# Optimization experiments

Hardware: AMD Instinct MI355X
Metric: run time of the kernel (lower is better)

## Reference

```python
import jax, jax.numpy as jnp
import numpy as np

ALPHA, BETA = 0.5, 0.25
DELTA_AGG, DELTA_DIS = 0.5, 3.0
OHEM_RATIO = 3
MAX_INST = 8  # instance ids in [0, MAX_INST); 0 = background
NEG_INF = -1e10


def _safe_norm(sq):
    # sqrt with zero-safe gradient; returns 0 where sq == 0
    return jnp.sqrt(jnp.where(sq > 0, sq, 1.0)) * (sq > 0)


def _agg_dis_single(sim, gt_text, gt_kernel):
    # sim: [4, N] float, gt_text/gt_kernel: [N] int32 instance ids
    lab = jnp.arange(1, MAX_INST)                                  # [K]
    kmask = (gt_kernel[None, :] == lab[:, None]).astype(sim.dtype)  # [K, N]
    tmask = gt_text[None, :] == lab[:, None]                        # [K, N] bool
    kcount = kmask.sum(1)
    tcount = tmask.sum(1).astype(sim.dtype)
    valid = (kcount > 0) & (tcount > 0)                             # [K]
    # per-instance kernel centroid G_kernel: masked segment mean of sim vectors
    G = (kmask @ sim.T) / jnp.maximum(kcount, 1.0)[:, None]         # [K, 4]
    # loss_agg: distance of each text pixel's sim vector to its kernel centroid
    diff = sim.T[None, :, :] - G[:, None, :]                        # [K, N, 4]
    d = _safe_norm(jnp.sum(diff * diff, -1))                        # [K, N]
    D = jnp.square(jnp.maximum(d - DELTA_AGG, 0.0))
    per_inst = jnp.sum(jnp.log1p(D) * tmask, 1) / jnp.maximum(tcount, 1.0)
    n_valid = jnp.sum(valid)
    loss_agg = jnp.sum(jnp.where(valid, per_inst, 0.0)) / jnp.maximum(n_valid, 1).astype(sim.dtype)
    # loss_dis: pairwise discrimination between valid kernel centroids
    gd = G[:, None, :] - G[None, :, :]                              # [K, K, 4]
    gnorm = _safe_norm(jnp.sum(gd * gd, -1))
    Dij = jnp.square(jnp.maximum(DELTA_DIS - gnorm, 0.0))
    K = MAX_INST - 1
    idx = jnp.arange(K)
    pair = valid[:, None] & valid[None, :] & (idx[:, None] < idx[None, :])
    s = jnp.sum(jnp.where(pair, jnp.log1p(Dij), 0.0))
    denom = (n_valid * (n_valid - 1)).astype(sim.dtype)  # matches torch: n*(n-1), not #pairs
    loss_dis = jnp.where(n_valid > 1, s / jnp.maximum(denom, 1.0), 0.0)
    return loss_agg, loss_dis


def _ohem_single(score, gt, tm):
    # score/tm: [N] float, gt: [N] int — all flattened
    pos = gt > 0.5
    pos_num = jnp.sum(pos) - jnp.sum(pos & (tm <= 0.5))
    neg = ~pos
    neg_total = jnp.sum(neg)
    neg_num = jnp.minimum(pos_num * OHEM_RATIO, neg_total)
    neg_scores = jnp.where(neg, score, NEG_INF)
    sorted_desc = -jnp.sort(-neg_scores)
    threshold = sorted_desc[jnp.maximum(neg_num - 1, 0)]
    sel = (((score >= threshold) | pos) & (tm > 0.5)).astype(tm.dtype)
    fallback = (pos_num == 0) | (neg_num == 0)
    return jnp.where(fallback, tm, sel)


def _dice(inp, tgt, mask):
    # inp: [B, N] logits, tgt: [B, N] (binarized at 0.5), mask: [B, N]
    p = jax.nn.sigmoid(inp) * mask
    t = (tgt > 0.5).astype(p.dtype) * mask
    a = jnp.sum(p * t, 1)
    b = jnp.sum(p * p, 1) + 1e-3
    c = jnp.sum(t * t, 1) + 1e-3
    return 1.0 - 2.0 * a / (b + c)


def _pan_loss(outputs, labels, training_masks):
    B = outputs.shape[0]
    texts = outputs[:, 0].reshape(B, -1)
    kernels = outputs[:, 1].reshape(B, -1)
    sim = outputs[:, 2:].reshape(B, 4, -1)
    gt_texts = labels[:, 0].reshape(B, -1)
    gt_kernels = labels[:, 1].reshape(B, -1)
    tm = training_masks.reshape(B, -1)

    loss_aggs, loss_diss = jax.vmap(_agg_dis_single)(sim, gt_texts, gt_kernels)

    # OHEM mask is computed on detached scores in the original (numpy round-trip)
    sel_text = jax.vmap(_ohem_single)(jax.lax.stop_gradient(texts), gt_texts, tm)
    loss_texts = _dice(texts, gt_texts, sel_text)

    sel_kernel = jax.lax.stop_gradient(
        ((jax.nn.sigmoid(texts) > 0.5) & (tm > 0.5)).astype(texts.dtype))
    loss_kernels = _dice(kernels, gt_kernels, sel_kernel)

    loss_text = loss_texts.mean()
    loss_kernel = loss_kernels.mean()
    loss_agg = loss_aggs.mean()
    loss_dis = loss_diss.mean()
    loss_all = loss_text + ALPHA * loss_kernel + BETA * (loss_agg + loss_dis)
    return loss_all, loss_text, loss_kernel, loss_agg, loss_dis


def setup_inputs() -> dict:
    key = jax.random.key(0)
    k1, k2, k3 = jax.random.split(key, 3)
    B, H, W = 8, 640, 640
    outputs = jax.random.normal(k1, (B, 6, H, W), dtype=jnp.float32)
    labels = jax.random.randint(k2, (B, 2, H, W), 0, MAX_INST).astype(jnp.int32)
    training_masks = jax.random.uniform(k3, (B, H, W), dtype=jnp.float32)
    return {"outputs": outputs, "labels": labels, "training_masks": training_masks}


def reference(outputs, labels, training_masks):
    return _pan_loss(outputs, labels, training_masks)
```

## Files before the change

kernel.cpp:

```cpp
#include <hip/hip_runtime.h>

#define NPIX 409600
#define NB 8

constexpr int OFF_H0   = 0;
constexpr int OFF_H1   = 2048;
constexpr int OFF_H2   = 4096;
constexpr int OFF_KC   = 5120;
constexpr int OFF_TC   = 5128;
constexpr int OFF_KS   = 5136;
constexpr int OFF_AGG  = 5168;
constexpr int OFF_CPOS = 5176;
constexpr int OFF_CPOSM= 5177;
constexpr int OFF_KN   = 5178;
constexpr int OFF_KNF  = 5179;
constexpr int OFF_FALL = 5180;
constexpr int OFF_NV   = 5181;
constexpr int OFF_VM   = 5182;
constexpr int OFF_LDIS = 5183;
constexpr int OFF_BTN  = 5184;
constexpr int OFF_PFX0 = 5185;
constexpr int OFF_K1   = 5186;
constexpr int OFF_PFX22= 5187;
constexpr int OFF_K2   = 5188;
constexpr int OFF_DICE = 5190;
constexpr int PER_BATCH= 5248;
constexpr int KEYS_BASE= NB * PER_BATCH;
constexpr int HDR_WORDS= NB * PER_BATCH;

__device__ __forceinline__ unsigned mapf(float s) {
  unsigned b = __float_as_uint(s);
  return (b & 0x80000000u) ? ~b : (b | 0x80000000u);
}
__device__ __forceinline__ float unmapf(unsigned u) {
  return __uint_as_float((u & 0x80000000u) ? (u & 0x7FFFFFFFu) : ~u);
}
__device__ __forceinline__ float wredf(float v) {
#pragma unroll
  for (int m = 32; m >= 1; m >>= 1) v += __shfl_xor(v, m, 64);
  return v;
}
__device__ __forceinline__ unsigned wredu(unsigned v) {
#pragma unroll
  for (int m = 32; m >= 1; m >>= 1) v += (unsigned)__shfl_xor((int)v, m, 64);
  return v;
}

__global__ __launch_bounds__(256) void kZ(unsigned* __restrict__ ws) {
  int i = blockIdx.x * 256 + threadIdx.x;
  if (i < HDR_WORDS) ws[i] = 0u;
}

__global__ __launch_bounds__(256) void kXS(const float* __restrict__ out_,
                                           const int* __restrict__ lab_,
                                           const float* __restrict__ tm_,
                                           unsigned* __restrict__ ws) {
  const int b = blockIdx.y;
  unsigned* wsb = ws + (size_t)b * PER_BATCH;
  float* wsbf = (float*)wsb;
  __shared__ __align__(16) unsigned shm[8508];
  const int tid = threadIdx.x, lane = tid & 63, w = tid >> 6;

  if (blockIdx.x < 200) {
    const int bx = blockIdx.x;
    unsigned* sh_h   = shm;
    unsigned* shScan = shm + 2048;
    unsigned* shTC   = shm + 2304;
    float*    shRed  = (float*)(shm + 2336);
    unsigned* shC    = shm + 2372;
    unsigned* shBase = shm + 2380;
    for (int i = tid; i < 2048; i += 256) sh_h[i] = 0u;
    __syncthreads();

    const float4* tx = (const float4*)(out_ + (size_t)b * 6 * NPIX);
    const float4* kr = (const float4*)(out_ + (size_t)b * 6 * NPIX + (size_t)NPIX);
    const int4* gt = (const int4*)(lab_ + (size_t)b * 2 * NPIX);
    const int4* gk = (const int4*)(lab_ + (size_t)b * 2 * NPIX + NPIX);
    const float4* tmv = (const float4*)(tm_ + (size_t)b * NPIX);

    unsigned cpos = 0, cposm = 0, vmask = 0, fmask = 0;
    unsigned tcq[7];
#pragma unroll
    for (int k = 0; k < 7; ++k) tcq[k] = 0u;
    unsigned kreg[8];
    float at = 0.f, btp = 0.f, ct = 0.f, atf = 0.f, btf = 0.f, ctf = 0.f;
    float ak = 0.f, bk = 0.f, ck = 0.f;

#pragma unroll
    for (int it = 0; it < 2; ++it) {
      const int i = it * 51200 + bx * 256 + tid;
      float4 t4 = tx[i]; float4 q4 = kr[i]; int4 g4 = gt[i]; int4 k4 = gk[i]; float4 m4 = tmv[i];
#pragma unroll
      for (int j = 0; j < 4; ++j) {
        float tv = ((const float*)&t4)[j];
        float kv = ((const float*)&q4)[j];
        int gtv = ((const int*)&g4)[j];
        int gkv = ((const int*)&k4)[j];
        float mv = ((const float*)&m4)[j];
        bool pos = gtv > 0;
        bool mh = mv > 0.5f;
        cpos += pos;
        cposm += (pos && !mh);
        unsigned key = mapf(tv);
        kreg[it * 4 + j] = key;
        float sig = 1.f / (1.f + expf(-tv));
        if (!pos) {
          vmask |= 1u << (it * 4 + j);
          if (mh) fmask |= 1u << (it * 4 + j);
          atomicAdd(&sh_h[key >> 21], 1u);
        } else if (mh) {
          at += sig; btp += sig * sig; ct += 1.f;
        }
#pragma unroll
        for (int k = 0; k < 7; ++k)
          tcq[k] += (unsigned)__popcll(__ballot(gtv == k + 1));
        float sm = sig * mv;
        btf += sm * sm;
        if (pos) { atf += sm * mv; ctf += mv * mv; }
        if ((tv > 0.f) && mh) {
          float sk = 1.f / (1.f + expf(-kv));
          bk += sk * sk;
          if (gkv > 0) { ak += sk; ck += 1.f; }
        }
      }
    }

    unsigned r = wredu(cpos), r2 = wredu(cposm);
    if (lane == 0) { shC[w * 2] = r; shC[w * 2 + 1] = r2; }
    if (lane == 0) {
#pragma unroll
      for (int k = 0; k < 7; ++k) shTC[w * 7 + k] = tcq[k];
    }
    float v9[9] = {at, btp, ct, atf, btf, ctf, ak, bk, ck};
#pragma unroll
    for (int q = 0; q < 9; ++q) {
      float f = wredf(v9[q]);
      if (lane == 0) shRed[w * 9 + q] = f;
    }

    unsigned cnt = (unsigned)__popc(vmask), cntF = (unsigned)__popc(fmask);
    shScan[tid] = cnt | (cntF << 16);
    __syncthreads();
#pragma unroll
    for (int off = 1; off < 256; off <<= 1) {
      unsigned vv = (tid >= off) ? shScan[tid - off] : 0u;
      __syncthreads();
      shScan[tid] += vv;
      __syncthreads();
    }
    if (tid == 0) {
      unsigned tot = shScan[255];
      shBase[0] = atomicAdd(&wsb[OFF_KN], tot & 0xFFFFu);
      shBase[1] = atomicAdd(&wsb[OFF_KNF], tot >> 16);
    }
    for (int i = tid; i < 2048; i += 256) {
      unsigned h = sh_h[i]; if (h) atomicAdd(&wsb[OFF_H0 + i], h);
    }
    if (tid < 7) {
      unsigned s = shTC[tid] + shTC[7 + tid] + shTC[14 + tid] + shTC[21 + tid];
      if (s) atomicAdd(&wsb[OFF_TC + 1 + tid], s);
    } else if (tid >= 16 && tid < 25) {
      int q = tid - 16;
      float s = shRed[q] + shRed[9 + q] + shRed[18 + q] + shRed[27 + q];
      atomicAdd(&wsbf[OFF_DICE + q], s);
    } else if (tid == 30) {
      atomicAdd(&wsb[OFF_CPOS], shC[0] + shC[2] + shC[4] + shC[6]);
    } else if (tid == 31) {
      atomicAdd(&wsb[OFF_CPOSM], shC[1] + shC[3] + shC[5] + shC[7]);
    }
    __syncthreads();
    unsigned gA = shBase[0] + (shScan[tid] & 0xFFFFu) - cnt;
    unsigned gF = shBase[1] + (shScan[tid] >> 16) - cntF;
    unsigned* keys = ws + KEYS_BASE + (size_t)b * NPIX;
#pragma unroll
    for (int s = 0; s < 8; ++s)
      if (vmask & (1u << s)) { keys[gA] = kreg[s]; ++gA; }
#pragma unroll
    for (int s = 0; s < 8; ++s)
      if (fmask & (1u << s)) { keys[NPIX - 1 - gF] = kreg[s]; ++gF; }
  } else {
    const int bx = blockIdx.x - 200;
    float* L = (float*)shm;
    float* L2 = (float*)(shm + 8224);
    unsigned* sh_kcw = shm + 8480;
    for (int i = tid; i < 8224; i += 256) L[i] = 0.f;
    __syncthreads();

    const float4* s0 = (const float4*)(out_ + (size_t)b * 6 * NPIX + 2 * (size_t)NPIX);
    const float4* s1 = (const float4*)(out_ + (size_t)b * 6 * NPIX + 3 * (size_t)NPIX);
    const float4* s2 = (const float4*)(out_ + (size_t)b * 6 * NPIX + 4 * (size_t)NPIX);
    const float4* s3 = (const float4*)(out_ + (size_t)b * 6 * NPIX + 5 * (size_t)NPIX);
    const int4* gkk = (const int4*)(lab_ + (size_t)b * 2 * NPIX + NPIX);

    unsigned kcq[7];
#pragma unroll
    for (int k = 0; k < 7; ++k) kcq[k] = 0u;

    const int nv = NPIX / 4;
    for (int i = bx * 256 + tid; i < nv; i += 128 * 256) {
      int4 k4 = gkk[i];
      float4 a0 = s0[i], a1 = s1[i], a2 = s2[i], a3 = s3[i];
#pragma unroll
      for (int j = 0; j < 4; ++j) {
        int gkv = ((const int*)&k4)[j];
#pragma unroll
        for (int k = 0; k < 7; ++k)
          kcq[k] += (unsigned)__popcll(__ballot(gkv == k + 1));
        int idx = (gkv > 0) ? (gkv - 1) : 7;
        float4* slot = (float4*)&L[(idx * 257 + tid) * 4];
        float4 rr = *slot;
        rr.x += ((const float*)&a0)[j];
        rr.y += ((const float*)&a1)[j];
        rr.z += ((const float*)&a2)[j];
        rr.w += ((const float*)&a3)[j];
        *slot = rr;
      }
    }

    if (lane == 0) {
#pragma unroll
      for (int k = 0; k < 7; ++k) sh_kcw[w * 7 + k] = kcq[k];
    }
    __syncthreads();
    {
      int p = tid & 31, sub = tid >> 5;
      int idx = p & 7, c = p >> 3;
      float part = 0.f;
#pragma unroll
      for (int i = 0; i < 32; ++i) part += L[(idx * 257 + (sub + 8 * i)) * 4 + c];
      L2[p * 8 + sub] = part;
    }
    __syncthreads();
    if (tid < 32) {
      float s = 0.f;
#pragma unroll
      for (int q = 0; q < 8; ++q) s += L2[tid * 8 + q];
      int idx = tid & 7, c = tid >> 3;
      if (idx < 7 && s != 0.f) atomicAdd(&wsbf[OFF_KS + (idx + 1) * 4 + c], s);
    } else if (tid >= 64 && tid < 71) {
      int k = tid - 64;
      unsigned s = sh_kcw[k] + sh_kcw[7 + k] + sh_kcw[14 + k] + sh_kcw[21 + k];
      if (s) atomicAdd(&wsb[OFF_KC + 1 + k], s);
    }
  }
}

__global__ __launch_bounds__(256) void kGB(const float* __restrict__ out_,
                                           const int* __restrict__ lab_,
                                           unsigned* __restrict__ ws) {
  const int b = blockIdx.y;
  unsigned* wsb = ws + (size_t)b * PER_BATCH;
  float* wsbf = (float*)wsb;
  const int tid = threadIdx.x, lane = tid & 63, w = tid >> 6;

  if (blockIdx.x < 100) {
    __shared__ float sG[32];
    __shared__ float sAgg[4 * 7];
    const int bx = blockIdx.x;
    if (tid < 32) {
      int inst = tid >> 2, c = tid & 3;
      float g = 0.f;
      if (inst >= 1) {
        unsigned kc = wsb[OFF_KC + inst];
        g = wsbf[OFF_KS + inst * 4 + c] / fmaxf((float)kc, 1.f);
      }
      sG[tid] = g;
    }
    __syncthreads();
    const int4* gt = (const int4*)(lab_ + (size_t)b * 2 * NPIX);
    const float4* s0 = (const float4*)(out_ + (size_t)b * 6 * NPIX + 2 * (size_t)NPIX);
    const float4* s1 = (const float4*)(out_ + (size_t)b * 6 * NPIX + 3 * (size_t)NPIX);
    const float4* s2 = (const float4*)(out_ + (size_t)b * 6 * NPIX + 4 * (size_t)NPIX);
    const float4* s3 = (const float4*)(out_ + (size_t)b * 6 * NPIX + 5 * (size_t)NPIX);
    float agg[7];
#pragma unroll
    for (int k = 0; k < 7; ++k) agg[k] = 0.f;
#pragma unroll
    for (int it = 0; it < 4; ++it) {
      const int i = it * 25600 + bx * 256 + tid;
      int4 g4 = gt[i];
      float4 a0 = s0[i], a1 = s1[i], a2 = s2[i], a3 = s3[i];
#pragma unroll
      for (int j = 0; j < 4; ++j) {
        int gtv = ((const int*)&g4)[j];
        bool pos = gtv > 0;
        int kk = pos ? gtv : 0;
        float d0 = ((const float*)&a0)[j] - sG[kk * 4 + 0];
        float d1 = ((const float*)&a1)[j] - sG[kk * 4 + 1];
        float d2 = ((const float*)&a2)[j] - sG[kk * 4 + 2];
        float d3 = ((const float*)&a3)[j] - sG[kk * 4 + 3];
        float sq = d0 * d0 + d1 * d1 + d2 * d2 + d3 * d3;
        float d = (sq > 0.f) ? sqrtf(sq) : 0.f;
        float dd = fmaxf(d - 0.5f, 0.f);
        float lg = pos ? log1pf(dd * dd) : 0.f;
#pragma unroll
        for (int k = 0; k < 7; ++k) agg[k] += (gtv == k + 1) ? lg : 0.f;
      }
    }
#pragma unroll
    for (int k = 0; k < 7; ++k) {
      float f = wredf(agg[k]);
      if (lane == 0) sAgg[w * 7 + k] = f;
    }
    __syncthreads();
    if (tid < 7) {
      float s = sAgg[tid] + sAgg[7 + tid] + sAgg[14 + tid] + sAgg[21 + tid];
      if (s != 0.f) atomicAdd(&wsbf[OFF_AGG + 1 + tid], s);
    }
  } else {
    const int bb = blockIdx.x - 100;
    __shared__ unsigned S[256];
    __shared__ unsigned sh_h1[2048];
    __shared__ unsigned sh_k, sh_pfx0;
    __shared__ int sh_fall;
    if (tid == 0) {
      unsigned cpos = wsb[OFF_CPOS], cposm = wsb[OFF_CPOSM];
      long posnum = (long)cpos - (long)cposm;
      long cneg = (long)NPIX - (long)cpos;
      long negnum = posnum * 3; if (negnum > cneg) negnum = cneg;
      int fall = (posnum == 0) || (negnum == 0);
      wsb[OFF_FALL] = (unsigned)fall;
      sh_fall = fall; sh_k = (unsigned)negnum;
      float G[8][4];
      unsigned nvv = 0, vm = 0;
      for (int k = 1; k < 8; ++k) {
        unsigned kc = wsb[OFF_KC + k], tc = wsb[OFF_TC + k];
        float inv = 1.f / fmaxf((float)kc, 1.f);
        for (int c = 0; c < 4; ++c) G[k][c] = wsbf[OFF_KS + k * 4 + c] * inv;
        if (kc > 0 && tc > 0) { vm |= 1u << k; ++nvv; }
      }
      wsb[OFF_NV] = nvv; wsb[OFF_VM] = vm;
      float s = 0.f;
      for (int i = 1; i < 8; ++i) {
        if (!((vm >> i) & 1)) continue;
        for (int j = i + 1; j < 8; ++j) {
          if (!((vm >> j) & 1)) continue;
          float sq = 0.f;
          for (int c = 0; c < 4; ++c) { float d = G[i][c] - G[j][c]; sq += d * d; }
          float gn = (sq > 0.f) ? sqrtf(sq) : 0.f;
          float dd = fmaxf(3.0f - gn, 0.f);
          s += log1pf(dd * dd);
        }
      }
      float denom = (float)(nvv * (nvv > 0 ? nvv - 1u : 0u));
      wsbf[OFF_LDIS] = (nvv > 1) ? (s / fmaxf(denom, 1.f)) : 0.f;
    }
    __syncthreads();
    if (sh_fall) return;
    unsigned myp = 0;
#pragma unroll
    for (int j = 0; j < 8; ++j) myp += wsb[OFF_H0 + tid * 8 + j];
    S[tid] = myp;
    __syncthreads();
#pragma unroll
    for (int off = 1; off < 256; off <<= 1) {
      unsigned v = (tid + off < 256) ? S[tid + off] : 0u;
      __syncthreads();
      S[tid] += v;
      __syncthreads();
    }
    {
      unsigned k = sh_k;
      unsigned suf = S[tid], sufn = suf - myp;
      if (suf >= k && sufn < k) {
        unsigned kk = k - sufn;
        unsigned cum2 = 0; int bin = tid * 8;
#pragma unroll
        for (int j = 7; j >= 0; --j) {
          unsigned h = wsb[OFF_H0 + tid * 8 + j]; cum2 += h;
          if (cum2 >= kk) { bin = tid * 8 + j; kk -= (cum2 - h); break; }
        }
        sh_pfx0 = (unsigned)bin;
        wsb[OFF_PFX0] = (unsigned)bin;
        wsb[OFF_K1] = kk;
      }
    }
    __syncthreads();
    const unsigned pfx = sh_pfx0;
    const unsigned kn = wsb[OFF_KN];
    for (int i = tid; i < 2048; i += 256) sh_h1[i] = 0u;
    __syncthreads();
    const unsigned* keys = ws + KEYS_BASE + (size_t)b * NPIX;
    for (unsigned i = bb * 256u + tid; i < kn; i += 16u * 256u) {
      unsigned key = keys[i];
      if ((key >> 21) == pfx) atomicAdd(&sh_h1[(key >> 10) & 0x7FFu], 1u);
    }
    __syncthreads();
    for (int i = tid; i < 2048; i += 256) {
      unsigned v = sh_h1[i]; if (v) atomicAdd(&wsb[OFF_H1 + i], v);
    }
  }
}

__global__ __launch_bounds__(256) void kCD(unsigned* __restrict__ ws) {
  const int b = blockIdx.y;
  unsigned* wsb = ws + (size_t)b * PER_BATCH;
  if (wsb[OFF_FALL]) return;
  __shared__ unsigned S[256];
  __shared__ unsigned sh_h2[1024];
  __shared__ unsigned sh_p22;
  const int tid = threadIdx.x;
  unsigned myp = 0;
#pragma unroll
  for (int j = 0; j < 8; ++j) myp += wsb[OFF_H1 + tid * 8 + j];
  S[tid] = myp;
  __syncthreads();
#pragma unroll
  for (int off = 1; off < 256; off <<= 1) {
    unsigned v = (tid + off < 256) ? S[tid + off] : 0u;
    __syncthreads();
    S[tid] += v;
    __syncthreads();
  }
  {
    unsigned k = wsb[OFF_K1];
    unsigned suf = S[tid], sufn = suf - myp;
    if (suf >= k && sufn < k) {
      unsigned kk = k - sufn;
      unsigned cum2 = 0; int bin = tid * 8;
#pragma unroll
      for (int j = 7; j >= 0; --j) {
        unsigned h = wsb[OFF_H1 + tid * 8 + j]; cum2 += h;
        if (cum2 >= kk) { bin = tid * 8 + j; kk -= (cum2 - h); break; }
      }
      unsigned p22 = (wsb[OFF_PFX0] << 11) | (unsigned)bin;
      sh_p22 = p22;
      wsb[OFF_PFX22] = p22;
      wsb[OFF_K2] = kk;
    }
  }
  __syncthreads();
  const unsigned pfx22 = sh_p22;
  const unsigned kn = wsb[OFF_KN];
  for (int i = tid; i < 1024; i += 256) sh_h2[i] = 0u;
  __syncthreads();
  const unsigned* keys = ws + KEYS_BASE + (size_t)b * NPIX;
  for (unsigned i = blockIdx.x * 256u + tid; i < kn; i += 16u * 256u) {
    unsigned key = keys[i];
    if ((key >> 10) == pfx22) atomicAdd(&sh_h2[key & 0x3FFu], 1u);
  }
  __syncthreads();
  for (int i = tid; i < 1024; i += 256) {
    unsigned v = sh_h2[i]; if (v) atomicAdd(&wsb[OFF_H2 + i], v);
  }
}

__global__ __launch_bounds__(256) void kEF(unsigned* __restrict__ ws) {
  const int b = blockIdx.y;
  unsigned* wsb = ws + (size_t)b * PER_BATCH;
  float* wsbf = (float*)wsb;
  if (wsb[OFF_FALL]) return;
  __shared__ unsigned S[256];
  __shared__ unsigned sh_thk;
  __shared__ float sF[4];
  const int tid = threadIdx.x, lane = tid & 63, w = tid >> 6;
  unsigned myp = 0;
#pragma unroll
  for (int j = 0; j < 4; ++j) myp += wsb[OFF_H2 + tid * 4 + j];
  S[tid] = myp;
  __syncthreads();
#pragma unroll
  for (int off = 1; off < 256; off <<= 1) {
    unsigned v = (tid + off < 256) ? S[tid + off] : 0u;
    __syncthreads();
    S[tid] += v;
    __syncthreads();
  }
  {
    unsigned k = wsb[OFF_K2];
    unsigned suf = S[tid], sufn = suf - myp;
    if (suf >= k && sufn < k) {
      unsigned kk = k - sufn;
      unsigned cum2 = 0; int bin = tid * 4;
#pragma unroll
      for (int j = 3; j >= 0; --j) {
        unsigned h = wsb[OFF_H2 + tid * 4 + j]; cum2 += h;
        if (cum2 >= kk) { bin = tid * 4 + j; break; }
      }
      sh_thk = (wsb[OFF_PFX22] << 10) | (unsigned)bin;
    }
  }
  __syncthreads();
  const unsigned thkey = sh_thk;
  const unsigned knF = wsb[OFF_KNF];
  const unsigned* listB = ws + KEYS_BASE + (size_t)b * NPIX + (NPIX - knF);
  float part = 0.f;
  for (unsigned i = blockIdx.x * 256u + tid; i < knF; i += 16u * 256u) {
    unsigned key = listB[i];
    if (key >= thkey) {
      float tv = unmapf(key);
      float sg = 1.f / (1.f + expf(-tv));
      part += sg * sg;
    }
  }
  part = wredf(part);
  if (lane == 0) sF[w] = part;
  __syncthreads();
  if (tid == 0) {
    float s = sF[0] + sF[1] + sF[2] + sF[3];
    if (s != 0.f) atomicAdd(&wsbf[OFF_BTN], s);
  }
}

__global__ void kH(const unsigned* __restrict__ ws, float* __restrict__ out) {
  __shared__ float sv[4][8];
  const int b = threadIdx.x;
  if (b < 8) {
    const unsigned* wsb = ws + (size_t)b * PER_BATCH;
    const float* wsbf = (const float*)wsb;
    int fall = (int)wsb[OFF_FALL];
    float at, bt, ct;
    if (fall) {
      at = wsbf[OFF_DICE + 3]; bt = wsbf[OFF_DICE + 4]; ct = wsbf[OFF_DICE + 5];
    } else {
      at = wsbf[OFF_DICE + 0];
      bt = wsbf[OFF_DICE + 1] + wsbf[OFF_BTN];
      ct = wsbf[OFF_DICE + 2];
    }
    float lt = 1.f - 2.f * at / ((bt + 1e-3f) + (ct + 1e-3f));
    float ak = wsbf[OFF_DICE + 6], bk = wsbf[OFF_DICE + 7] + 1e-3f, ck = wsbf[OFF_DICE + 8] + 1e-3f;
    float lk = 1.f - 2.f * ak / (bk + ck);
    unsigned vm = wsb[OFF_VM], nvv = wsb[OFF_NV];
    float s = 0.f;
    for (int k = 1; k < 8; ++k)
      if ((vm >> k) & 1) s += wsbf[OFF_AGG + k] / fmaxf((float)wsb[OFF_TC + k], 1.f);
    float la = s / fmaxf((float)nvv, 1.f);
    float ld = wsbf[OFF_LDIS];
    sv[0][b] = lt; sv[1][b] = lk; sv[2][b] = la; sv[3][b] = ld;
  }
  __syncthreads();
  if (threadIdx.x == 0) {
    float mt = 0.f, mk = 0.f, ma = 0.f, md = 0.f;
    for (int i = 0; i < 8; ++i) { mt += sv[0][i]; mk += sv[1][i]; ma += sv[2][i]; md += sv[3][i]; }
    mt *= 0.125f; mk *= 0.125f; ma *= 0.125f; md *= 0.125f;
    out[0] = mt + 0.5f * mk + 0.25f * (ma + md);
    out[1] = mt;
    out[2] = mk;
    out[3] = ma;
    out[4] = md;
  }
}

extern "C" void kernel_launch(void* const* d_in, const int* in_sizes, int n_in,
                              void* d_out, int out_size, void* d_ws, size_t ws_size,
                              hipStream_t stream) {
  const float* outputs = (const float*)d_in[0];
  const int* labels = (const int*)d_in[1];
  const float* tm = (const float*)d_in[2];
  unsigned* ws = (unsigned*)d_ws;
  float* out = (float*)d_out;

  dim3 blk(256);
  kZ<<<(HDR_WORDS + 255) / 256, blk, 0, stream>>>(ws);
  kXS<<<dim3(328, NB), blk, 0, stream>>>(outputs, labels, tm, ws);
  kGB<<<dim3(116, NB), blk, 0, stream>>>(outputs, labels, ws);
  kCD<<<dim3(16, NB), blk, 0, stream>>>(ws);
  kEF<<<dim3(16, NB), blk, 0, stream>>>(ws);
  kH<<<1, 64, 0, stream>>>(ws, out);
}
```

Before: 97.60 us.

## Split centroid accumulation across channel pairs, widen agg grid, use fast math intrinsics

The kernel-centroid accumulation blocks in kXS now each handle two of the four similarity channels, doubling that block count and halving per-block shared memory (and so the whole kernel's LDS footprint), which should raise occupancy. The aggregation part of kGB now runs with twice as many blocks, each doing half the iterations. Sigmoid and log1p move to __expf/__fdividef/__logf intrinsics, which are cheaper but less accurate and could shift the loss slightly. The label grid is now read twice by the split centroid blocks.

```diff
diff --git a/kernel.cpp b/kernel.cpp
--- a/kernel.cpp
+++ b/kernel.cpp
@@ -35,6 +35,9 @@
 __device__ __forceinline__ float unmapf(unsigned u) {
   return __uint_as_float((u & 0x80000000u) ? (u & 0x7FFFFFFFu) : ~u);
 }
+__device__ __forceinline__ float sigf(float x) {
+  return __fdividef(1.f, 1.f + __expf(-x));
+}
 __device__ __forceinline__ float wredf(float v) {
 #pragma unroll
   for (int m = 32; m >= 1; m >>= 1) v += __shfl_xor(v, m, 64);
@@ -58,7 +61,7 @@
   const int b = blockIdx.y;
   unsigned* wsb = ws + (size_t)b * PER_BATCH;
   float* wsbf = (float*)wsb;
-  __shared__ __align__(16) unsigned shm[8508];
+  __shared__ __align__(16) unsigned shm[4412];
   const int tid = threadIdx.x, lane = tid & 63, w = tid >> 6;
 
   if (blockIdx.x < 200) {
@@ -103,7 +106,7 @@
         cposm += (pos && !mh);
         unsigned key = mapf(tv);
         kreg[it * 4 + j] = key;
-        float sig = 1.f / (1.f + expf(-tv));
+        float sig = sigf(tv);
         if (!pos) {
           vmask |= 1u << (it * 4 + j);
           if (mh) fmask |= 1u << (it * 4 + j);
@@ -118,7 +121,7 @@
         btf += sm * sm;
         if (pos) { atf += sm * mv; ctf += mv * mv; }
         if ((tv > 0.f) && mh) {
-          float sk = 1.f / (1.f + expf(-kv));
+          float sk = sigf(kv);
           bk += sk * sk;
           if (gkv > 0) { ak += sk; ck += 1.f; }
         }
@@ -179,17 +182,16 @@
     for (int s = 0; s < 8; ++s)
       if (fmask & (1u << s)) { keys[NPIX - 1 - gF] = kreg[s]; ++gF; }
   } else {
-    const int bx = blockIdx.x - 200;
+    const bool lo = blockIdx.x < 328;
+    const int bx = lo ? (blockIdx.x - 200) : (blockIdx.x - 328);
     float* L = (float*)shm;
-    float* L2 = (float*)(shm + 8224);
-    unsigned* sh_kcw = shm + 8480;
-    for (int i = tid; i < 8224; i += 256) L[i] = 0.f;
-    __syncthreads();
-
-    const float4* s0 = (const float4*)(out_ + (size_t)b * 6 * NPIX + 2 * (size_t)NPIX);
-    const float4* s1 = (const float4*)(out_ + (size_t)b * 6 * NPIX + 3 * (size_t)NPIX);
-    const float4* s2 = (const float4*)(out_ + (size_t)b * 6 * NPIX + 4 * (size_t)NPIX);
-    const float4* s3 = (const float4*)(out_ + (size_t)b * 6 * NPIX + 5 * (size_t)NPIX);
+    float* L2 = (float*)(shm + 4112);
+    unsigned* sh_kcw = shm + 4384;
+    for (int i = tid; i < 4112; i += 256) L[i] = 0.f;
+    __syncthreads();
+
+    const float4* sa = (const float4*)(out_ + (size_t)b * 6 * NPIX + (size_t)(lo ? 2 : 4) * NPIX);
+    const float4* sb = (const float4*)(out_ + (size_t)b * 6 * NPIX + (size_t)(lo ? 3 : 5) * NPIX);
     const int4* gkk = (const int4*)(lab_ + (size_t)b * 2 * NPIX + NPIX);
 
     unsigned kcq[7];
@@ -199,45 +201,46 @@
     const int nv = NPIX / 4;
     for (int i = bx * 256 + tid; i < nv; i += 128 * 256) {
       int4 k4 = gkk[i];
-      float4 a0 = s0[i], a1 = s1[i], a2 = s2[i], a3 = s3[i];
+      float4 a0 = sa[i], a1 = sb[i];
 #pragma unroll
       for (int j = 0; j < 4; ++j) {
         int gkv = ((const int*)&k4)[j];
-#pragma unroll
-        for (int k = 0; k < 7; ++k)
-          kcq[k] += (unsigned)__popcll(__ballot(gkv == k + 1));
+        if (lo) {
+#pragma unroll
+          for (int k = 0; k < 7; ++k)
+            kcq[k] += (unsigned)__popcll(__ballot(gkv == k + 1));
+        }
         int idx = (gkv > 0) ? (gkv - 1) : 7;
-        float4* slot = (float4*)&L[(idx * 257 + tid) * 4];
-        float4 rr = *slot;
+        float2* slot = (float2*)&L[(idx * 257 + tid) * 2];
+        float2 rr = *slot;
         rr.x += ((const float*)&a0)[j];
         rr.y += ((const float*)&a1)[j];
-        rr.z += ((const float*)&a2)[j];
-        rr.w += ((const float*)&a3)[j];
         *slot = rr;
       }
     }
 
-    if (lane == 0) {
+    if (lo && lane == 0) {
 #pragma unroll
       for (int k = 0; k < 7; ++k) sh_kcw[w * 7 + k] = kcq[k];
     }
     __syncthreads();
     {
-      int p = tid & 31, sub = tid >> 5;
-      int idx = p & 7, c = p >> 3;
+      int p = tid & 15, sub = tid >> 4;
+      int idx = p & 7, c = (p >> 3) & 1;
       float part = 0.f;
 #pragma unroll
-      for (int i = 0; i < 32; ++i) part += L[(idx * 257 + (sub + 8 * i)) * 4 + c];
-      L2[p * 8 + sub] = part;
-    }
-    __syncthreads();
-    if (tid < 32) {
+      for (int q = 0; q < 16; ++q) part += L[(idx * 257 + (sub + 16 * q)) * 2 + c];
+      L2[p * 17 + sub] = part;
+    }
+    __syncthreads();
+    if (tid < 16) {
       float s = 0.f;
 #pragma unroll
-      for (int q = 0; q < 8; ++q) s += L2[tid * 8 + q];
-      int idx = tid & 7, c = tid >> 3;
-      if (idx < 7 && s != 0.f) atomicAdd(&wsbf[OFF_KS + (idx + 1) * 4 + c], s);
-    } else if (tid >= 64 && tid < 71) {
+      for (int q = 0; q < 16; ++q) s += L2[tid * 17 + q];
+      int idx = tid & 7, c = (tid >> 3) & 1;
+      if (idx < 7 && s != 0.f)
+        atomicAdd(&wsbf[OFF_KS + (idx + 1) * 4 + (lo ? 0 : 2) + c], s);
+    } else if (lo && tid >= 64 && tid < 71) {
       int k = tid - 64;
       unsigned s = sh_kcw[k] + sh_kcw[7 + k] + sh_kcw[14 + k] + sh_kcw[21 + k];
       if (s) atomicAdd(&wsb[OFF_KC + 1 + k], s);
@@ -253,7 +256,7 @@
   float* wsbf = (float*)wsb;
   const int tid = threadIdx.x, lane = tid & 63, w = tid >> 6;
 
-  if (blockIdx.x < 100) {
+  if (blockIdx.x < 200) {
     __shared__ float sG[32];
     __shared__ float sAgg[4 * 7];
     const int bx = blockIdx.x;
@@ -276,8 +279,8 @@
 #pragma unroll
     for (int k = 0; k < 7; ++k) agg[k] = 0.f;
 #pragma unroll
-    for (int it = 0; it < 4; ++it) {
-      const int i = it * 25600 + bx * 256 + tid;
+    for (int it = 0; it < 2; ++it) {
+      const int i = it * 51200 + bx * 256 + tid;
       int4 g4 = gt[i];
       float4 a0 = s0[i], a1 = s1[i], a2 = s2[i], a3 = s3[i];
 #pragma unroll
@@ -292,7 +295,7 @@
         float sq = d0 * d0 + d1 * d1 + d2 * d2 + d3 * d3;
         float d = (sq > 0.f) ? sqrtf(sq) : 0.f;
         float dd = fmaxf(d - 0.5f, 0.f);
-        float lg = pos ? log1pf(dd * dd) : 0.f;
+        float lg = pos ? __logf(1.f + dd * dd) : 0.f;
 #pragma unroll
         for (int k = 0; k < 7; ++k) agg[k] += (gtv == k + 1) ? lg : 0.f;
       }
@@ -308,7 +311,7 @@
       if (s != 0.f) atomicAdd(&wsbf[OFF_AGG + 1 + tid], s);
     }
   } else {
-    const int bb = blockIdx.x - 100;
+    const int bb = blockIdx.x - 200;
     __shared__ unsigned S[256];
     __shared__ unsigned sh_h1[2048];
     __shared__ unsigned sh_k, sh_pfx0;
@@ -488,8 +491,7 @@
   for (unsigned i = blockIdx.x * 256u + tid; i < knF; i += 16u * 256u) {
     unsigned key = listB[i];
     if (key >= thkey) {
-      float tv = unmapf(key);
-      float sg = 1.f / (1.f + expf(-tv));
+      float sg = sigf(unmapf(key));
       part += sg * sg;
     }
   }
@@ -552,8 +554,8 @@
 
   dim3 blk(256);
   kZ<<<(HDR_WORDS + 255) / 256, blk, 0, stream>>>(ws);
-  kXS<<<dim3(328, NB), blk, 0, stream>>>(outputs, labels, tm, ws);
-  kGB<<<dim3(116, NB), blk, 0, stream>>>(outputs, labels, ws);
+  kXS<<<dim3(456, NB), blk, 0, stream>>>(outputs, labels, tm, ws);
+  kGB<<<dim3(216, NB), blk, 0, stream>>>(outputs, labels, ws);
   kCD<<<dim3(16, NB), blk, 0, stream>>>(ws);
   kEF<<<dim3(16, NB), blk, 0, stream>>>(ws);
   kH<<<1, 64, 0, stream>>>(ws, out);
```

After: 88.54 us. -9.3%, faster.
